# Kernel optimization log

Hardware: AMD Instinct MI355X
Metric: run time of the kernel (lower is better)

## Reference

```python
import jax, jax.numpy as jnp
import numpy as np

K = 3  # kernel_size

def setup_inputs() -> dict:
    key = jax.random.key(0)
    ks = jax.random.split(key, 7)
    B, C, H, W = 4, 128, 128, 128
    MID = int(C * 0.2)  # 25
    return {
        "x":  jax.random.normal(ks[0], (B, C, H, W), dtype=jnp.float32),
        "Ws": jax.random.normal(ks[1], (K * K, C), dtype=jnp.float32) * 0.1,
        "bs": jax.random.normal(ks[2], (K * K,), dtype=jnp.float32) * 0.1,
        "W1": jax.random.normal(ks[3], (MID, C), dtype=jnp.float32) * 0.1,
        "b1": jax.random.normal(ks[4], (MID,), dtype=jnp.float32) * 0.1,
        "W2": jax.random.normal(ks[5], (C * K * K, MID), dtype=jnp.float32) * 0.1,
        "b2": jax.random.normal(ks[6], (C * K * K,), dtype=jnp.float32) * 0.1,
    }

def reference(x, Ws, bs, W1, b1, W2, b2):
    b, c, h, w = x.shape
    k = K
    # channel branch: global avg pool -> 1x1 conv -> relu -> 1x1 conv -> sigmoid
    xm = x.mean(axis=(2, 3))                                   # [b, c]
    hid = jax.nn.relu(xm @ W1.T + b1)                          # [b, mid]
    channel_filter = jax.nn.sigmoid(hid @ W2.T + b2)           # [b, c*k*k]
    channel_filter = channel_filter.reshape(b, c, k * k, 1, 1)
    # spatial branch: 1x1 conv C -> k*k, sigmoid
    spatial_filter = jax.nn.sigmoid(
        jnp.einsum('bchw,oc->bohw', x, Ws) + bs[None, :, None, None]
    ).reshape(b, 1, k * k, h, w)
    filt = spatial_filter * channel_filter                     # [b, c, k*k, h, w]
    # unfold (k=3, pad=1, stride=1, dilation=1): stack 9 shifted views
    xp = jnp.pad(x, ((0, 0), (0, 0), (1, 1), (1, 1)))
    patches = jnp.stack(
        [xp[:, :, i:i + h, j:j + w] for i in range(k) for j in range(k)],
        axis=2,
    )  # [b, c, k*k, h, w] — matches nn.Unfold's (c, k*k) ordering
    return (patches * filt).sum(axis=2)                        # [b, c, h, w]
```

## Files before the change

kernel.cpp:

```cpp
#include <hip/hip_runtime.h>

#define B 4
#define C 128
#define H 128
#define W 128
#define HW (H * W)
#define KK 9
#define MID 25

#define SPATIAL_BLKS (HW / 64)

#define WS_XM 0
#define WS_S  8192

__global__ __launch_bounds__(256) void k_ms(
    const float* __restrict__ x, const float* __restrict__ Ws,
    const float* __restrict__ bs, float* __restrict__ xm,
    float* __restrict__ S)
{
    __shared__ float red[3 * KK * 64];
    const int b = blockIdx.y;

    if (blockIdx.x >= SPATIAL_BLKS) {
        const int c = blockIdx.x - SPATIAL_BLKS;
        const float4* plane = (const float4*)(x + ((size_t)b * C + c) * HW);
        float s = 0.0f;
#pragma unroll
        for (int i = 0; i < 16; ++i) {
            float4 v = plane[i * 256 + threadIdx.x];
            s += (v.x + v.y) + (v.z + v.w);
        }
#pragma unroll
        for (int off = 32; off > 0; off >>= 1) s += __shfl_down(s, off, 64);
        if ((threadIdx.x & 63) == 0) red[threadIdx.x >> 6] = s;
        __syncthreads();
        if (threadIdx.x == 0)
            xm[b * C + c] = ((red[0] + red[1]) + (red[2] + red[3])) * (1.0f / HW);
        return;
    }

    const int lane = threadIdx.x & 63;
    const int wave = threadIdx.x >> 6;
    const int p = blockIdx.x * 64 + lane;
    const float* xb = x + (size_t)b * C * HW + p;

    float acc[KK];
#pragma unroll
    for (int k = 0; k < KK; ++k) acc[k] = (wave == 0) ? bs[k] : 0.0f;

    const int cbase = wave * 32;
#pragma unroll
    for (int i = 0; i < 32; ++i) {
        const int c = cbase + i;
        float v = xb[(size_t)c * HW];
#pragma unroll
        for (int k = 0; k < KK; ++k)
            acc[k] = fmaf(v, Ws[k * C + c], acc[k]);
    }

    if (wave > 0) {
#pragma unroll
        for (int k = 0; k < KK; ++k)
            red[((wave - 1) * KK + k) * 64 + lane] = acc[k];
    }
    __syncthreads();
    if (wave == 0) {
#pragma unroll
        for (int k = 0; k < KK; ++k) {
            float a = acc[k] + red[(0 * KK + k) * 64 + lane]
                             + red[(1 * KK + k) * 64 + lane]
                             + red[(2 * KK + k) * 64 + lane];
            S[((size_t)(b * KK + k)) * HW + p] = 1.0f / (1.0f + __expf(-a));
        }
    }
}

__global__ __launch_bounds__(256) void k_conv(
    const float* __restrict__ x, const float* __restrict__ S,
    const float* __restrict__ xm,
    const float* __restrict__ W1, const float* __restrict__ b1,
    const float* __restrict__ W2, const float* __restrict__ b2,
    float* __restrict__ out)
{
    const int tid = threadIdx.x;
    const int b = blockIdx.y;
    const int c0 = blockIdx.z * (C / 16);

    __shared__ float xmean[C];
    __shared__ float hid[MID];
    __shared__ float chs[(C / 16) * KK];
    if (tid < C) xmean[tid] = xm[b * C + tid];
    __syncthreads();
    if (tid < MID) {
        float a = b1[tid];
#pragma unroll 8
        for (int c = 0; c < C; ++c)
            a = fmaf(xmean[c], W1[tid * C + c], a);
        hid[tid] = fmaxf(a, 0.0f);
    }
    __syncthreads();
    if (tid < (C / 16) * KK) {
        const int o = c0 * KK + tid;
        float a = b2[o];
#pragma unroll
        for (int m = 0; m < MID; ++m)
            a = fmaf(hid[m], W2[o * MID + m], a);
        chs[tid] = 1.0f / (1.0f + __expf(-a));
    }
    __syncthreads();

    const int p0 = (blockIdx.x * 256 + tid) * 4;
    const int h = p0 >> 7;
    const int w0 = p0 & (W - 1);

    float4 sv[KK];
    const float* Sb = S + (size_t)b * KK * HW + p0;
#pragma unroll
    for (int k = 0; k < KK; ++k) {
        const int di = k / 3 - 1, dj = k % 3 - 1;
        const int hh = h + di;
        float4 s4 = *(const float4*)(Sb + (size_t)k * HW);
        if (hh < 0 || hh >= H) s4 = make_float4(0.f, 0.f, 0.f, 0.f);
        if (dj == -1 && w0 == 0)     s4.x = 0.f;
        if (dj == +1 && w0 == W - 4) s4.w = 0.f;
        sv[k] = s4;
    }

    const int r0 = max(h - 1, 0), r2 = min(h + 1, H - 1);
    const int rowoff[3] = { r0 * W + w0, h * W + w0, r2 * W + w0 };
    const int loff = (w0 > 0) ? -1 : 0;
    const int roff = (w0 < W - 4) ? 4 : 0;

    const float* xb = x + (size_t)b * C * HW;
    float* ob = out + (size_t)b * C * HW + p0;

    for (int ci = 0; ci < C / 16; ++ci) {
        const int c = c0 + ci;
        const float* xc = xb + (size_t)c * HW;
        float4 Cx[3];
        float  Lw[3], Rx[3];
#pragma unroll
        for (int r = 0; r < 3; ++r) {
            const float* bp = xc + rowoff[r];
            Cx[r] = *(const float4*)bp;
            Lw[r] = bp[loff];
            Rx[r] = bp[roff];
        }
        float4 a = make_float4(0.f, 0.f, 0.f, 0.f);
#pragma unroll
        for (int k = 0; k < KK; ++k) {
            const int r = k / 3, dj = k % 3 - 1;
            float4 t;
            if (dj == -1)     t = make_float4(Lw[r], Cx[r].x, Cx[r].y, Cx[r].z);
            else if (dj == 0) t = Cx[r];
            else              t = make_float4(Cx[r].y, Cx[r].z, Cx[r].w, Rx[r]);
            const float cf = chs[ci * KK + k];
            a.x = fmaf(t.x, sv[k].x * cf, a.x);
            a.y = fmaf(t.y, sv[k].y * cf, a.y);
            a.z = fmaf(t.z, sv[k].z * cf, a.z);
            a.w = fmaf(t.w, sv[k].w * cf, a.w);
        }
        *(float4*)(ob + (size_t)c * HW) = a;
    }
}

extern "C" void kernel_launch(void* const* d_in, const int* in_sizes, int n_in,
                              void* d_out, int out_size, void* d_ws, size_t ws_size,
                              hipStream_t stream) {
    (void)in_sizes; (void)n_in; (void)out_size; (void)ws_size;
    const float* x  = (const float*)d_in[0];
    const float* Ws = (const float*)d_in[1];
    const float* bs = (const float*)d_in[2];
    const float* W1 = (const float*)d_in[3];
    const float* b1 = (const float*)d_in[4];
    const float* W2 = (const float*)d_in[5];
    const float* b2 = (const float*)d_in[6];
    float* out = (float*)d_out;
    float* ws  = (float*)d_ws;

    float* xm = ws + WS_XM;
    float* S  = ws + WS_S;

    k_ms<<<dim3(SPATIAL_BLKS + C, B), 256, 0, stream>>>(x, Ws, bs, xm, S);
    k_conv<<<dim3(HW / 1024, B, 16), 256, 0, stream>>>(x, S, xm, W1, b1, W2, b2, out);
}
```

Measured before the change: 123.2 us.

## Vectorize spatial projection, parallelize hidden MLP, use nontemporal output stores

The spatial 1x1-conv kernel now has each thread process four pixels with float4 loads and accumulators, so each block covers 256 pixels and there are four times fewer blocks. The per-block hidden-layer computation in the conv kernel is split across 250 threads that produce partial sums, followed by a small reduction, which shortens the serial prologue. Output stores use nontemporal writes to avoid polluting the cache. In exchange, register pressure in k_ms rises from the 36 float accumulators, and shared memory grows fourfold.

```diff
diff --git a/kernel.cpp b/kernel.cpp
--- a/kernel.cpp
+++ b/kernel.cpp
@@ -8,7 +8,9 @@
 #define KK 9
 #define MID 25
 
-#define SPATIAL_BLKS (HW / 64)
+#define SPATIAL_BLKS (HW / 256)
+
+typedef float nat_f4 __attribute__((ext_vector_type(4)));
 
 #define WS_XM 0
 #define WS_S  8192
@@ -18,7 +20,8 @@
     const float* __restrict__ bs, float* __restrict__ xm,
     float* __restrict__ S)
 {
-    __shared__ float red[3 * KK * 64];
+    __shared__ float4 red4[3 * KK * 64];
+    __shared__ float redm[4];
     const int b = blockIdx.y;
 
     if (blockIdx.x >= SPATIAL_BLKS) {
@@ -32,45 +35,63 @@
         }
 #pragma unroll
         for (int off = 32; off > 0; off >>= 1) s += __shfl_down(s, off, 64);
-        if ((threadIdx.x & 63) == 0) red[threadIdx.x >> 6] = s;
+        if ((threadIdx.x & 63) == 0) redm[threadIdx.x >> 6] = s;
         __syncthreads();
         if (threadIdx.x == 0)
-            xm[b * C + c] = ((red[0] + red[1]) + (red[2] + red[3])) * (1.0f / HW);
+            xm[b * C + c] = ((redm[0] + redm[1]) + (redm[2] + redm[3])) * (1.0f / HW);
         return;
     }
 
     const int lane = threadIdx.x & 63;
     const int wave = threadIdx.x >> 6;
-    const int p = blockIdx.x * 64 + lane;
-    const float* xb = x + (size_t)b * C * HW + p;
-
-    float acc[KK];
-#pragma unroll
-    for (int k = 0; k < KK; ++k) acc[k] = (wave == 0) ? bs[k] : 0.0f;
+    const int p0 = blockIdx.x * 256 + lane * 4;
+    const float4* xb = (const float4*)(x + (size_t)b * C * HW + p0);
+
+    float4 acc[KK];
+#pragma unroll
+    for (int k = 0; k < KK; ++k) {
+        const float bk = (wave == 0) ? bs[k] : 0.0f;
+        acc[k] = make_float4(bk, bk, bk, bk);
+    }
 
     const int cbase = wave * 32;
 #pragma unroll
     for (int i = 0; i < 32; ++i) {
         const int c = cbase + i;
-        float v = xb[(size_t)c * HW];
+        float4 v = xb[(size_t)c * (HW / 4)];
+#pragma unroll
+        for (int k = 0; k < KK; ++k) {
+            const float wk = Ws[k * C + c];
+            acc[k].x = fmaf(v.x, wk, acc[k].x);
+            acc[k].y = fmaf(v.y, wk, acc[k].y);
+            acc[k].z = fmaf(v.z, wk, acc[k].z);
+            acc[k].w = fmaf(v.w, wk, acc[k].w);
+        }
+    }
+
+    if (wave > 0) {
 #pragma unroll
         for (int k = 0; k < KK; ++k)
-            acc[k] = fmaf(v, Ws[k * C + c], acc[k]);
-    }
-
-    if (wave > 0) {
-#pragma unroll
-        for (int k = 0; k < KK; ++k)
-            red[((wave - 1) * KK + k) * 64 + lane] = acc[k];
+            red4[((wave - 1) * KK + k) * 64 + lane] = acc[k];
     }
     __syncthreads();
     if (wave == 0) {
 #pragma unroll
         for (int k = 0; k < KK; ++k) {
-            float a = acc[k] + red[(0 * KK + k) * 64 + lane]
-                             + red[(1 * KK + k) * 64 + lane]
-                             + red[(2 * KK + k) * 64 + lane];
-            S[((size_t)(b * KK + k)) * HW + p] = 1.0f / (1.0f + __expf(-a));
+            float4 a = acc[k];
+            float4 r0 = red4[(0 * KK + k) * 64 + lane];
+            float4 r1 = red4[(1 * KK + k) * 64 + lane];
+            float4 r2 = red4[(2 * KK + k) * 64 + lane];
+            a.x += (r0.x + r1.x) + r2.x;
+            a.y += (r0.y + r1.y) + r2.y;
+            a.z += (r0.z + r1.z) + r2.z;
+            a.w += (r0.w + r1.w) + r2.w;
+            float4 sg;
+            sg.x = 1.0f / (1.0f + __expf(-a.x));
+            sg.y = 1.0f / (1.0f + __expf(-a.y));
+            sg.z = 1.0f / (1.0f + __expf(-a.z));
+            sg.w = 1.0f / (1.0f + __expf(-a.w));
+            *(float4*)(S + ((size_t)(b * KK + k)) * HW + p0) = sg;
         }
     }
 }
@@ -87,15 +108,24 @@
     const int c0 = blockIdx.z * (C / 16);
 
     __shared__ float xmean[C];
+    __shared__ float hpart[MID * 10];
     __shared__ float hid[MID];
     __shared__ float chs[(C / 16) * KK];
     if (tid < C) xmean[tid] = xm[b * C + tid];
     __syncthreads();
+    if (tid < MID * 10) {
+        const int m = tid / 10, seg = tid % 10;
+        const int cb = seg * 13, ce = (cb + 13 < C) ? cb + 13 : C;
+        float a = 0.0f;
+        for (int c = cb; c < ce; ++c)
+            a = fmaf(xmean[c], W1[m * C + c], a);
+        hpart[tid] = a;
+    }
+    __syncthreads();
     if (tid < MID) {
         float a = b1[tid];
-#pragma unroll 8
-        for (int c = 0; c < C; ++c)
-            a = fmaf(xmean[c], W1[tid * C + c], a);
+#pragma unroll
+        for (int s = 0; s < 10; ++s) a += hpart[tid * 10 + s];
         hid[tid] = fmaxf(a, 0.0f);
     }
     __syncthreads();
@@ -160,7 +190,8 @@
             a.z = fmaf(t.z, sv[k].z * cf, a.z);
             a.w = fmaf(t.w, sv[k].w * cf, a.w);
         }
-        *(float4*)(ob + (size_t)c * HW) = a;
+        nat_f4 av = { a.x, a.y, a.z, a.w };
+        __builtin_nontemporal_store(av, (nat_f4*)(ob + (size_t)c * HW));
     }
 }
 
```

After: 124.2 us. No clear change (+0.8%).
